# Optimization experiments

Hardware: AMD Instinct MI355X
Metric: run time of the kernel (lower is better)

Reference implementation:

```python
import math
import jax, jax.numpy as jnp
import numpy as np

B, LD, LE = 8, 512, 512
D, H, DK, F, L, V = 1024, 16, 64, 4096, 3, 32000
EPS = 1e-5
NEG = -1000000000.0


def setup_inputs() -> dict:
    key = jax.random.key(0)
    ks = jax.random.split(key, 16)
    s = 0.02
    dec_inputs = jax.random.randint(ks[0], (B, LD), 0, V)
    # causal mask: True = masked out (matches masked_fill semantics)
    self_mask = jnp.broadcast_to(jnp.triu(jnp.ones((LD, LD), bool), k=1), (B, LD, LD))
    enc_output = jax.random.normal(ks[1], (B, LE, D), jnp.float32)
    encoder_mask = jnp.zeros((B, LD, LE), bool)  # no encoder padding
    embed = jax.random.normal(ks[2], (V, D), jnp.float32) * s
    # sinusoidal positional encoding, pe[:LD]
    pos = jnp.arange(LD, dtype=jnp.float32)[:, None]
    div = jnp.exp(jnp.arange(0, D, 2, dtype=jnp.float32) * (-math.log(10000.0) / D))
    pe = jnp.zeros((LD, D), jnp.float32)
    pe = pe.at[:, 0::2].set(jnp.sin(pos * div)).at[:, 1::2].set(jnp.cos(pos * div))
    # per-layer params; axis 1 of attn params: 0=self-attn, 1=enc-dec attn
    wq = jax.random.normal(ks[3], (L, 2, D, D), jnp.float32) * s
    wk = jax.random.normal(ks[4], (L, 2, D, D), jnp.float32) * s
    wv = jax.random.normal(ks[5], (L, 2, D, D), jnp.float32) * s
    wo = jax.random.normal(ks[6], (L, 2, D, D), jnp.float32) * s
    bq = jnp.zeros((L, 2, D), jnp.float32)
    bk = jnp.zeros((L, 2, D), jnp.float32)
    bv = jnp.zeros((L, 2, D), jnp.float32)
    bo = jnp.zeros((L, 2, D), jnp.float32)
    ffn_w1 = jax.random.normal(ks[7], (L, F, D), jnp.float32) * s
    ffn_b1 = jnp.zeros((L, F), jnp.float32)
    ffn_w2 = jax.random.normal(ks[8], (L, D, F), jnp.float32) * s
    ffn_b2 = jnp.zeros((L, D), jnp.float32)
    ln_g = jnp.ones((L, 3, D), jnp.float32)   # norm1/2/3 gains
    ln_b = jnp.zeros((L, 3, D), jnp.float32)  # norm1/2/3 biases
    return dict(dec_inputs=dec_inputs, self_mask=self_mask, enc_output=enc_output,
                encoder_mask=encoder_mask, embed=embed, pe=pe,
                wq=wq, bq=bq, wk=wk, bk=bk, wv=wv, bv=bv, wo=wo, bo=bo,
                ffn_w1=ffn_w1, ffn_b1=ffn_b1, ffn_w2=ffn_w2, ffn_b2=ffn_b2,
                ln_g=ln_g, ln_b=ln_b)


def _ln(x, g, b):
    m = jnp.mean(x, axis=-1, keepdims=True)
    v = jnp.mean((x - m) ** 2, axis=-1, keepdims=True)
    return (x - m) * jax.lax.rsqrt(v + EPS) * g + b


def _mha(qi, ki, vi, mask, wq, bq, wk, bk, wv, bv, wo, bo):
    Bq, Lq, _ = qi.shape
    Lk = ki.shape[1]
    Q = (qi @ wq.T + bq).reshape(Bq, Lq, H, DK).transpose(0, 2, 1, 3)
    K = (ki @ wk.T + bk).reshape(Bq, Lk, H, DK).transpose(0, 2, 1, 3)
    Vv = (vi @ wv.T + bv).reshape(Bq, Lk, H, DK).transpose(0, 2, 1, 3)
    scores = jnp.einsum('bhqd,bhkd->bhqk', Q, K) / math.sqrt(DK)
    scores = jnp.where(mask[:, None, :, :], NEG, scores)
    attn = jax.nn.softmax(scores, axis=-1)
    ctx = jnp.einsum('bhqk,bhkd->bhqd', attn, Vv)
    ctx = ctx.transpose(0, 2, 1, 3).reshape(Bq, Lq, H * DK)
    return ctx @ wo.T + bo


def reference(dec_inputs, self_mask, enc_output, encoder_mask, embed, pe,
              wq, bq, wk, bk, wv, bv, wo, bo,
              ffn_w1, ffn_b1, ffn_w2, ffn_b2, ln_g, ln_b):
    x = embed[dec_inputs] * math.sqrt(D) + pe[None, :, :]
    for l in range(L):
        h = _ln(x, ln_g[l, 0], ln_b[l, 0])
        a = _mha(h, h, h, self_mask,
                 wq[l, 0], bq[l, 0], wk[l, 0], bk[l, 0], wv[l, 0], bv[l, 0], wo[l, 0], bo[l, 0])
        x = x + a
        h = _ln(x, ln_g[l, 1], ln_b[l, 1])
        c = _mha(h, enc_output, enc_output, encoder_mask,
                 wq[l, 1], bq[l, 1], wk[l, 1], bk[l, 1], wv[l, 1], bv[l, 1], wo[l, 1], bo[l, 1])
        x = x + c
        h = _ln(x, ln_g[l, 2], ln_b[l, 2])
        f = jax.nn.relu(h @ ffn_w1[l].T + ffn_b1[l]) @ ffn_w2[l].T + ffn_b2[l]
        # faithful quirk of the source: residual is the cross-attn output, not x
        x = c + f
    return x
```

## Files before the change

kernel.cpp:

```cpp
#include <hip/hip_runtime.h>
#include <hip/hip_bf16.h>

using bf16x8 = __attribute__((ext_vector_type(8))) short;
using f32x4  = __attribute__((ext_vector_type(4))) float;
using u16x4  = __attribute__((ext_vector_type(4))) unsigned short;

#define DEVI static __device__ __forceinline__
#define SBAR() asm volatile("s_barrier" ::: "memory")

DEVI unsigned short f2b(float f) {
  unsigned int u = __float_as_uint(f);
  u += 0x7FFFu + ((u >> 16) & 1u);
  return (unsigned short)(u >> 16);
}

DEVI void gload16(const unsigned short* g, unsigned short* l) {
  __builtin_amdgcn_global_load_lds(
      (const __attribute__((address_space(1))) unsigned int*)g,
      (__attribute__((address_space(3))) unsigned int*)l, 16, 0, 0);
}

DEVI float wred_max16(float v) {
#pragma unroll
  for (int m = 1; m < 16; m <<= 1) v = fmaxf(v, __shfl_xor(v, m, 64));
  return v;
}
DEVI float wred_sum16(float v) {
#pragma unroll
  for (int m = 1; m < 16; m <<= 1) v += __shfl_xor(v, m, 64);
  return v;
}


__global__ void cvt_kernel(const float* __restrict__ in,
                           unsigned short* __restrict__ out, int n4) {
  int i = blockIdx.x * blockDim.x + threadIdx.x;
  const int stride = gridDim.x * blockDim.x;
  for (; i < n4; i += stride) {
    const float4 v = ((const float4*)in)[i];
    u16x4 o;
    o[0] = f2b(v.x); o[1] = f2b(v.y); o[2] = f2b(v.z); o[3] = f2b(v.w);
    ((u16x4*)out)[i] = o;
  }
}

__global__ void pack_w(const float* __restrict__ s0,
                       const float* __restrict__ s1,
                       const float* __restrict__ s2,
                       int sub, unsigned short* __restrict__ dst, int nm) {
  const int r = blockIdx.x;
  const int m = blockIdx.y;
  const int l = blockIdx.z;
  const float* src = (m == 0 ? s0 : m == 1 ? s1 : s2)
                   + (size_t)(l * 2 + sub) * 1048576 + (size_t)r * 1024;
  unsigned short* d = dst + ((size_t)(l * nm + m) * 1024 + r) * 1024;
  const int col = threadIdx.x * 4;
  const float4 v = *(const float4*)(src + col);
  u16x4 o;
  o[0] = f2b(v.x); o[1] = f2b(v.y); o[2] = f2b(v.z); o[3] = f2b(v.w);
  *(u16x4*)(d + col) = o;
}

__global__ void pack_bias(const float* __restrict__ s0,
                          const float* __restrict__ s1,
                          const float* __restrict__ s2,
                          int sub, float* __restrict__ dst, int nm) {
  const int m = blockIdx.x, l = blockIdx.y;
  const float* src = (m == 0 ? s0 : m == 1 ? s1 : s2) + (size_t)(l * 2 + sub) * 1024;
  float* d = dst + ((size_t)l * nm + m) * 1024;
  const int i = threadIdx.x * 4;
  *(float4*)(d + i) = *(const float4*)(src + i);
}

__global__ void embed_kernel(const int* __restrict__ ids,
                             const float* __restrict__ emb,
                             const float* __restrict__ pe,
                             float* __restrict__ x) {
  const int row = blockIdx.x;
  const int t = row & 511;
  const int col = threadIdx.x * 4;
  const int id = ids[row];
  const float4 e = *(const float4*)(emb + (size_t)id * 1024 + col);
  const float4 p = *(const float4*)(pe + (size_t)t * 1024 + col);
  float4 o;
  o.x = e.x * 32.f + p.x; o.y = e.y * 32.f + p.y;
  o.z = e.z * 32.f + p.z; o.w = e.w * 32.f + p.w;
  *(float4*)(x + (size_t)row * 1024 + col) = o;
}

__global__ void ln_kernel(const float* __restrict__ x,
                          const float* __restrict__ g,
                          const float* __restrict__ b,
                          unsigned short* __restrict__ out) {
  const int row = blockIdx.x;
  const int l = threadIdx.x;
  const float4* xr = (const float4*)(x + (size_t)row * 1024);
  float4 v[4];
  float s = 0.f;
#pragma unroll
  for (int i = 0; i < 4; ++i) {
    v[i] = xr[l * 4 + i];
    s += v[i].x + v[i].y + v[i].z + v[i].w;
  }
#pragma unroll
  for (int m = 1; m < 64; m <<= 1) s += __shfl_xor(s, m, 64);
  const float mean = s * (1.f / 1024.f);
  float vs = 0.f;
#pragma unroll
  for (int i = 0; i < 4; ++i) {
    float dx = v[i].x - mean, dy = v[i].y - mean, dz = v[i].z - mean, dw = v[i].w - mean;
    vs += dx * dx + dy * dy + dz * dz + dw * dw;
  }
#pragma unroll
  for (int m = 1; m < 64; m <<= 1) vs += __shfl_xor(vs, m, 64);
  const float inv = rsqrtf(vs * (1.f / 1024.f) + 1e-5f);
#pragma unroll
  for (int i = 0; i < 4; ++i) {
    const int col = l * 16 + i * 4;
    const float4 gg = *(const float4*)(g + col);
    const float4 bb = *(const float4*)(b + col);
    u16x4 o;
    o[0] = f2b((v[i].x - mean) * inv * gg.x + bb.x);
    o[1] = f2b((v[i].y - mean) * inv * gg.y + bb.y);
    o[2] = f2b((v[i].z - mean) * inv * gg.z + bb.z);
    o[3] = f2b((v[i].w - mean) * inv * gg.w + bb.w);
    *(u16x4*)(out + (size_t)row * 1024 + col) = o;
  }
}

__global__ void reduce4_ln_kernel(const float* __restrict__ c,
                                  const float* __restrict__ pbuf,
                                  const float* __restrict__ bias,
                                  const float* __restrict__ g,
                                  const float* __restrict__ e,
                                  float* __restrict__ x,
                                  unsigned short* __restrict__ hb) {
  const int row = blockIdx.x;
  const int l = threadIdx.x;
  const size_t base = (size_t)row * 1024;
  const float4* cc = (const float4*)(c + base);
  const float4* p0 = (const float4*)(pbuf + base);
  const float4* p1 = (const float4*)(pbuf + 4194304 + base);
  const float4* p2 = (const float4*)(pbuf + 2 * 4194304 + base);
  const float4* p3 = (const float4*)(pbuf + 3 * 4194304 + base);
  float4 v[4];
  float s = 0.f;
#pragma unroll
  for (int i = 0; i < 4; ++i) {
    const int fi = l * 4 + i;
    const float4 a = cc[fi];
    const float4 b0 = p0[fi], b1 = p1[fi], b2v = p2[fi], b3 = p3[fi];
    const float4 bb = ((const float4*)bias)[fi & 255];
    float4 o;
    o.x = a.x + (b0.x + b1.x) + (b2v.x + b3.x) + bb.x;
    o.y = a.y + (b0.y + b1.y) + (b2v.y + b3.y) + bb.y;
    o.z = a.z + (b0.z + b1.z) + (b2v.z + b3.z) + bb.z;
    o.w = a.w + (b0.w + b1.w) + (b2v.w + b3.w) + bb.w;
    v[i] = o;
    s += o.x + o.y + o.z + o.w;
    *(float4*)(x + base + fi * 4) = o;
  }
#pragma unroll
  for (int m = 1; m < 64; m <<= 1) s += __shfl_xor(s, m, 64);
  const float mean = s * (1.f / 1024.f);
  float vs = 0.f;
#pragma unroll
  for (int i = 0; i < 4; ++i) {
    float dx = v[i].x - mean, dy = v[i].y - mean, dz = v[i].z - mean, dw = v[i].w - mean;
    vs += dx * dx + dy * dy + dz * dz + dw * dw;
  }
#pragma unroll
  for (int m = 1; m < 64; m <<= 1) vs += __shfl_xor(vs, m, 64);
  const float inv = rsqrtf(vs * (1.f / 1024.f) + 1e-5f);
#pragma unroll
  for (int i = 0; i < 4; ++i) {
    const int col = l * 16 + i * 4;
    const float4 gg = *(const float4*)(g + col);
    const float4 bb = *(const float4*)(e + col);
    u16x4 o;
    o[0] = f2b((v[i].x - mean) * inv * gg.x + bb.x);
    o[1] = f2b((v[i].y - mean) * inv * gg.y + bb.y);
    o[2] = f2b((v[i].z - mean) * inv * gg.z + bb.z);
    o[3] = f2b((v[i].w - mean) * inv * gg.w + bb.w);
    *(u16x4*)(hb + base + col) = o;
  }
}


template<int LDA, int LDB>
DEVI void gemm8p_core(const unsigned short* __restrict__ A,
                      const unsigned short* __restrict__ Bw,
                      int m0, int n0, int kofs,
                      unsigned short* AsE, unsigned short* BsE,
                      unsigned short* AsO, unsigned short* BsO,
                      int tid, f32x4 (&acc)[8][4]) {
  constexpr int NT = 16;
  const int lane = tid & 63;
  const int wave = tid >> 6;
  const int wr = wave >> 2;
  const int wc = wave & 3;
  const int ro = lane & 15;
  const int hi = lane >> 4;

  auto stA = [&](unsigned short* buf, int q, int kt) {
    const int row = tid >> 3;
    const int lc = (tid & 7) ^ (row & 7);
    gload16(A + (size_t)(m0 + q * 64 + row) * LDA + kofs + kt * 64 + lc * 8,
            buf + q * 4096 + tid * 8);
  };
  auto stB = [&](unsigned short* buf, int q, int kt) {
    const int row = tid >> 3;
    const int lc = (tid & 7) ^ (row & 7);
    gload16(Bw + (size_t)(n0 + q * 64 + row) * LDB + kofs + kt * 64 + lc * 8,
            buf + q * 4096 + tid * 8);
  };

  bf16x8 af[4][2], bfL[2][2], bfR[2][2];
  auto ldAL = [&](const unsigned short* buf) {
#pragma unroll
    for (int mi = 0; mi < 4; ++mi) {
      const int r = wr * 128 + mi * 16 + ro;
#pragma unroll
      for (int ks = 0; ks < 2; ++ks)
        af[mi][ks] = *(const bf16x8*)&buf[r * 64 + (((ks << 2) + hi) ^ (r & 7)) * 8];
    }
  };
  auto ldAH = [&](const unsigned short* buf) {
#pragma unroll
    for (int mi = 0; mi < 4; ++mi) {
      const int r = wr * 128 + 64 + mi * 16 + ro;
#pragma unroll
      for (int ks = 0; ks < 2; ++ks)
        af[mi][ks] = *(const bf16x8*)&buf[r * 64 + (((ks << 2) + hi) ^ (r & 7)) * 8];
    }
  };
  auto ldBL = [&](const unsigned short* buf) {
#pragma unroll
    for (int nj = 0; nj < 2; ++nj) {
      const int r = wc * 64 + nj * 16 + ro;
#pragma unroll
      for (int ks = 0; ks < 2; ++ks)
        bfL[nj][ks] = *(const bf16x8*)&buf[r * 64 + (((ks << 2) + hi) ^ (r & 7)) * 8];
    }
  };
  auto ldBR = [&](const unsigned short* buf) {
#pragma unroll
    for (int nj = 0; nj < 2; ++nj) {
      const int r = wc * 64 + 32 + nj * 16 + ro;
#pragma unroll
      for (int ks = 0; ks < 2; ++ks)
        bfR[nj][ks] = *(const bf16x8*)&buf[r * 64 + (((ks << 2) + hi) ^ (r & 7)) * 8];
    }
  };
  auto mmQ = [&](bf16x8 (&bf)[2][2], int mo, int no) {
    __builtin_amdgcn_s_setprio(1);
#pragma unroll
    for (int ks = 0; ks < 2; ++ks)
#pragma unroll
      for (int mi = 0; mi < 4; ++mi)
#pragma unroll
        for (int nj = 0; nj < 2; ++nj)
          acc[mo + mi][no + nj] =
              __builtin_amdgcn_mfma_f32_16x16x32_bf16(af[mi][ks], bf[nj][ks],
                                                      acc[mo + mi][no + nj], 0, 0, 0);
    __builtin_amdgcn_s_setprio(0);
  };

  stA(AsE, 0, 0); stA(AsE, 1, 0); stA(AsE, 2, 0); stA(AsE, 3, 0);
  stB(BsE, 0, 0); stB(BsE, 1, 0); stB(BsE, 2, 0); stB(BsE, 3, 0);
  stA(AsO, 0, 1); stA(AsO, 1, 1); stA(AsO, 2, 1); stA(AsO, 3, 1);
  stB(BsO, 0, 1); stB(BsO, 1, 1);
  asm volatile("s_waitcnt vmcnt(0)" ::: "memory");
  SBAR();

  for (int t = 0; t < NT; t += 2) {
    const bool last = (t + 2 >= NT);
    ldAL(AsE); ldBL(BsE);
    stB(BsO, 2, t + 1); stB(BsO, 3, t + 1);
    SBAR(); mmQ(bfL, 0, 0); SBAR();
    ldBR(BsE);
    if (!last) { stA(AsE, 0, t + 2); stA(AsE, 2, t + 2); }
    SBAR(); mmQ(bfR, 0, 2); SBAR();
    ldAH(AsE);
    if (!last) { stB(BsE, 0, t + 2); stB(BsE, 1, t + 2); }
    SBAR(); mmQ(bfL, 4, 0); SBAR();
    if (!last) {
      stA(AsE, 1, t + 2); stA(AsE, 3, t + 2);
      asm volatile("s_waitcnt vmcnt(6)" ::: "memory");
    } else {
      asm volatile("s_waitcnt vmcnt(0)" ::: "memory");
    }
    SBAR(); mmQ(bfR, 4, 2); SBAR();
    ldAL(AsO); ldBL(BsO);
    if (!last) { stB(BsE, 2, t + 2); stB(BsE, 3, t + 2); }
    SBAR(); mmQ(bfL, 0, 0); SBAR();
    ldBR(BsO);
    if (!last) { stA(AsO, 0, t + 3); stA(AsO, 2, t + 3); }
    SBAR(); mmQ(bfR, 0, 2); SBAR();
    ldAH(AsO);
    if (!last) { stB(BsO, 0, t + 3); stB(BsO, 1, t + 3); }
    SBAR(); mmQ(bfL, 4, 0); SBAR();
    if (!last) {
      stA(AsO, 1, t + 3); stA(AsO, 3, t + 3);
      asm volatile("s_waitcnt vmcnt(6)" ::: "memory");
    }
    SBAR(); mmQ(bfR, 4, 2); SBAR();
  }
}

template<int EPI, int VT>
__global__ __launch_bounds__(512, 1) void gemm8p(
    const unsigned short* __restrict__ A,
    const unsigned short* __restrict__ Bw,
    const float* __restrict__ bias,
    int N, unsigned short* __restrict__ out0,
    unsigned short* __restrict__ vt) {
  __shared__ alignas(16) unsigned short AsE[256 * 64];
  __shared__ alignas(16) unsigned short BsE[256 * 64];
  __shared__ alignas(16) unsigned short AsO[256 * 64];
  __shared__ alignas(16) unsigned short BsO[256 * 64];
  const int tid = threadIdx.x;
  int id = blockIdx.x;
  const int nwg = gridDim.x;
  id = (id & 7) * (nwg >> 3) + (id >> 3);
  const int nn = N >> 8;
  const int bx = id % nn;
  const int by = id / nn;
  const int m0 = by * 256;
  const int n0 = bx * 256;

  f32x4 acc[8][4];
#pragma unroll
  for (int i = 0; i < 8; ++i)
#pragma unroll
    for (int j = 0; j < 4; ++j) acc[i][j] = f32x4{0.f, 0.f, 0.f, 0.f};

  gemm8p_core<1024, 1024>(A, Bw, m0, n0, 0, AsE, BsE, AsO, BsO, tid, acc);

  const int lane = tid & 63;
  const int wave = tid >> 6;
  const int wr = wave >> 2, wc = wave & 3;
  const int ro = lane & 15, hi = lane >> 4;
  const int r4 = hi * 4;
#pragma unroll
  for (int mi = 0; mi < 8; ++mi) {
#pragma unroll
    for (int nj = 0; nj < 4; ++nj) {
      const int cg = n0 + wc * 64 + nj * 16 + ro;
      const float bv = bias[cg];
      const int rg0 = m0 + wr * 128 + mi * 16 + r4;
      const bool isV1 = (VT == 1) && (cg >= 2048);
      const bool isV2 = (VT == 2) && ((cg & 2047) >= 1024);
      if (isV1 || isV2) {
        u16x4 o;
#pragma unroll
        for (int q = 0; q < 4; ++q) o[q] = f2b(acc[mi][nj][q] + bv);
        const int b = rg0 >> 9, t = rg0 & 511;
        size_t dst;
        if (isV1) {
          const int hh = (cg - 2048) >> 6, d = (cg - 2048) & 63;
          dst = (((size_t)(b * 16 + hh) * 64 + d) << 9) + t;
        } else {
          const int layer = cg >> 11;
          const int cm = (cg & 2047) - 1024;
          dst = (size_t)layer * 4194304 +
                (((size_t)(b * 16 + (cm >> 6)) * 64 + (cm & 63)) << 9) + t;
        }
        *(u16x4*)&vt[dst] = o;
      } else {
#pragma unroll
        for (int q = 0; q < 4; ++q) {
          const float v = acc[mi][nj][q] + bv;
          out0[(size_t)(rg0 + q) * N + cg] = f2b(EPI == 1 ? fmaxf(v, 0.f) : v);
        }
      }
    }
  }
}

__global__ __launch_bounds__(512, 1) void gemm_sk8(
    const unsigned short* __restrict__ A,
    const unsigned short* __restrict__ Bw,
    float* __restrict__ pbuf) {
  __shared__ alignas(16) unsigned short AsE[256 * 64];
  __shared__ alignas(16) unsigned short BsE[256 * 64];
  __shared__ alignas(16) unsigned short AsO[256 * 64];
  __shared__ alignas(16) unsigned short BsO[256 * 64];
  const int tid = threadIdx.x;
  int id = blockIdx.x;
  const int nwg = gridDim.x;
  id = (id & 7) * (nwg >> 3) + (id >> 3);
  const int s  = id >> 6;
  const int r6 = id & 63;
  const int bx = r6 & 3;
  const int by = r6 >> 2;
  const int m0 = by * 256;
  const int n0 = bx * 256;

  f32x4 acc[8][4];
#pragma unroll
  for (int i = 0; i < 8; ++i)
#pragma unroll
    for (int j = 0; j < 4; ++j) acc[i][j] = f32x4{0.f, 0.f, 0.f, 0.f};

  gemm8p_core<4096, 4096>(A, Bw, m0, n0, s * 1024, AsE, BsE, AsO, BsO, tid, acc);

  float* out = pbuf + (size_t)s * 4096 * 1024;
  const int lane = tid & 63;
  const int wave = tid >> 6;
  const int wr = wave >> 2, wc = wave & 3;
  const int ro = lane & 15, hi = lane >> 4;
  const int r4 = hi * 4;
#pragma unroll
  for (int mi = 0; mi < 8; ++mi)
#pragma unroll
    for (int nj = 0; nj < 4; ++nj) {
      const int cg = n0 + wc * 64 + nj * 16 + ro;
#pragma unroll
      for (int q = 0; q < 4; ++q) {
        const int rg = m0 + wr * 128 + mi * 16 + r4 + q;
        out[(size_t)rg * 1024 + cg] = acc[mi][nj][q];
      }
    }
}

__global__ void reduce4_kernel(const float* __restrict__ c,
                               const float* __restrict__ pbuf,
                               const float* __restrict__ bias,
                               float* __restrict__ xout) {
  const int n4 = 4096 * 1024 / 4;
  int i = blockIdx.x * blockDim.x + threadIdx.x;
  const int stride = gridDim.x * blockDim.x;
  const float4* p0 = (const float4*)pbuf;
  const float4* p1 = (const float4*)(pbuf + 4194304);
  const float4* p2 = (const float4*)(pbuf + 2 * 4194304);
  const float4* p3 = (const float4*)(pbuf + 3 * 4194304);
  for (; i < n4; i += stride) {
    const float4 cc = ((const float4*)c)[i];
    const float4 a0 = p0[i];
    const float4 a1 = p1[i];
    const float4 a2 = p2[i];
    const float4 a3 = p3[i];
    const float4 bb = ((const float4*)bias)[i & 255];
    float4 o;
    o.x = cc.x + (a0.x + a1.x) + (a2.x + a3.x) + bb.x;
    o.y = cc.y + (a0.y + a1.y) + (a2.y + a3.y) + bb.y;
    o.z = cc.z + (a0.z + a1.z) + (a2.z + a3.z) + bb.z;
    o.w = cc.w + (a0.w + a1.w) + (a2.w + a3.w) + bb.w;
    ((float4*)xout)[i] = o;
  }
}


enum { EPI_BF16 = 0, EPI_RELU_BF16 = 1, EPI_RES = 2, EPI_RES2 = 3 };

template<int EPI, int BM, int BN>
__global__ void gemm_bt(const unsigned short* __restrict__ A,
                        const unsigned short* __restrict__ Bw,
                        const float* __restrict__ bias,
                        int N, int K, int nn,
                        void* out0, const float* res, float* out1) {
  constexpr int MI = BM / 32;
  constexpr int NJ = BN / 32;
  __shared__ alignas(16) unsigned short As[2][BM * 64];
  __shared__ alignas(16) unsigned short Bs[2][BN * 64];
  const int tid = threadIdx.x;
  const int lane = tid & 63;
  const int wave = tid >> 6;
  int id = blockIdx.x;
  const int nwg = gridDim.x;
  id = (id & 7) * (nwg >> 3) + (id >> 3);
  const int bx = id % nn;
  const int by = id / nn;
  const int m0 = by * BM;
  const int n0 = bx * BN;
  const int wm = (wave >> 1) * (BM / 2);
  const int wn = (wave & 1) * (BN / 2);

  auto stage = [&](int buf, int kt) {
    const size_t k0 = (size_t)kt * 64;
#pragma unroll
    for (int i = 0; i < MI; ++i) {
      const int c = tid + 256 * i;
      const int row = c >> 3;
      const int lc = (c & 7) ^ (row & 7);
      gload16(A + (size_t)(m0 + row) * K + k0 + lc * 8, &As[buf][c * 8]);
    }
#pragma unroll
    for (int i = 0; i < NJ; ++i) {
      const int c = tid + 256 * i;
      const int row = c >> 3;
      const int lc = (c & 7) ^ (row & 7);
      gload16(Bw + (size_t)(n0 + row) * K + k0 + lc * 8, &Bs[buf][c * 8]);
    }
  };

  f32x4 acc[MI][NJ];
#pragma unroll
  for (int i = 0; i < MI; ++i)
#pragma unroll
    for (int j = 0; j < NJ; ++j) acc[i][j] = f32x4{0.f, 0.f, 0.f, 0.f};

  const int nk = K >> 6;
  stage(0, 0);
  int cur = 0;
  const int ro = lane & 15;
  const int hi = lane >> 4;
  for (int kt = 0; kt < nk; ++kt) {
    __syncthreads();
    if (kt + 1 < nk) stage(cur ^ 1, kt + 1);
    bf16x8 af[MI][2], bf[NJ][2];
#pragma unroll
    for (int i = 0; i < MI; ++i) {
      const int r = wm + i * 16 + ro;
#pragma unroll
      for (int ks = 0; ks < 2; ++ks)
        af[i][ks] = *(const bf16x8*)&As[cur][r * 64 + (((ks << 2) + hi) ^ (r & 7)) * 8];
    }
#pragma unroll
    for (int j = 0; j < NJ; ++j) {
      const int r = wn + j * 16 + ro;
#pragma unroll
      for (int ks = 0; ks < 2; ++ks)
        bf[j][ks] = *(const bf16x8*)&Bs[cur][r * 64 + (((ks << 2) + hi) ^ (r & 7)) * 8];
    }
#pragma unroll
    for (int ks = 0; ks < 2; ++ks)
#pragma unroll
      for (int i = 0; i < MI; ++i)
#pragma unroll
        for (int j = 0; j < NJ; ++j)
          acc[i][j] = __builtin_amdgcn_mfma_f32_16x16x32_bf16(af[i][ks], bf[j][ks], acc[i][j], 0, 0, 0);
    cur ^= 1;
  }

  const int r4 = hi * 4;
#pragma unroll
  for (int i = 0; i < MI; ++i) {
#pragma unroll
    for (int j = 0; j < NJ; ++j) {
      const int cg = n0 + wn + j * 16 + ro;
      const float bv = bias[cg];
#pragma unroll
      for (int q = 0; q < 4; ++q) {
        const int rg = m0 + wm + i * 16 + r4 + q;
        const size_t idx = (size_t)rg * N + cg;
        const float v = acc[i][j][q] + bv;
        if (EPI == EPI_BF16) {
          ((unsigned short*)out0)[idx] = f2b(v);
        } else if (EPI == EPI_RELU_BF16) {
          ((unsigned short*)out0)[idx] = f2b(fmaxf(v, 0.f));
        } else if (EPI == EPI_RES) {
          ((float*)out0)[idx] = res[idx] + v;
        } else {
          const float r = res[idx];
          ((float*)out0)[idx] = v;
          out1[idx] = r + v;
        }
      }
    }
  }
}


template<bool CAUSAL>
__global__ __launch_bounds__(256) void attn_kernel(
    const unsigned short* __restrict__ Qg, int qs,
    const unsigned short* __restrict__ Kg, int ksd,
    const unsigned short* __restrict__ Vt,
    unsigned short* __restrict__ Og) {
  __shared__ alignas(16) unsigned short Ks[2][64 * 64];
  __shared__ alignas(16) unsigned short Vs[2][64 * 64];
  __shared__ alignas(16) unsigned short Pl[4][32 * 64];
  const int qt0 = blockIdx.x;
  const int h  = blockIdx.y;
  const int b  = blockIdx.z;
  const int tid = threadIdx.x;
  const int lane = tid & 63;
  const int w = tid >> 6;
  const int ro = lane & 15;
  const int hi = lane >> 4;
  const int qrow0 = qt0 * 128 + w * 32;
  const size_t qbase = (size_t)b * 512 * qs  + (size_t)h * 64;
  const size_t kbase = (size_t)b * 512 * ksd + (size_t)h * 64;
  const size_t vbase = ((size_t)(b * 16 + h)) * 64 * 512;
  const size_t obase = (size_t)b * 512 * 1024 + (size_t)h * 64;

  bf16x8 qf[2][2];
#pragma unroll
  for (int mi = 0; mi < 2; ++mi)
#pragma unroll
    for (int ks = 0; ks < 2; ++ks)
      qf[mi][ks] = *(const bf16x8*)&Qg[qbase + (size_t)(qrow0 + mi * 16 + ro) * qs + ks * 32 + hi * 8];

  f32x4 o[2][4];
  float mrun[2][4], lrun[2][4];
#pragma unroll
  for (int mi = 0; mi < 2; ++mi) {
#pragma unroll
    for (int di = 0; di < 4; ++di) o[mi][di] = f32x4{0.f, 0.f, 0.f, 0.f};
#pragma unroll
    for (int q = 0; q < 4; ++q) { mrun[mi][q] = -1e30f; lrun[mi][q] = 0.f; }
  }

  auto stage = [&](int buf, int kt) {
#pragma unroll
    for (int i = 0; i < 2; ++i) {
      const int c = tid + 256 * i;
      const int row = c >> 3;
      const int lc = (c & 7) ^ (row & 7);
      gload16(Kg + kbase + (size_t)(kt * 64 + row) * ksd + lc * 8, &Ks[buf][c * 8]);
    }
#pragma unroll
    for (int i = 0; i < 2; ++i) {
      const int c = tid + 256 * i;
      const int row = c >> 3;
      const int lc = (c & 7) ^ (row & 7);
      gload16(Vt + vbase + (size_t)row * 512 + (size_t)kt * 64 + lc * 8, &Vs[buf][c * 8]);
    }
  };

  const int ktmax = CAUSAL ? (qt0 * 2 + 1) : 7;
  stage(0, 0);
  int cur = 0;
  for (int kt = 0; kt <= ktmax; ++kt) {
    __syncthreads();
    if (kt < ktmax) stage(cur ^ 1, kt + 1);
    const bool skip = CAUSAL && (kt * 64 > qrow0 + 31);
    if (!skip) {
      bf16x8 kf[4][2];
#pragma unroll
      for (int ni = 0; ni < 4; ++ni) {
        const int r = ni * 16 + ro;
#pragma unroll
        for (int ks = 0; ks < 2; ++ks)
          kf[ni][ks] = *(const bf16x8*)&Ks[cur][r * 64 + (((ks << 2) + hi) ^ (r & 7)) * 8];
      }

      f32x4 s[2][4];
#pragma unroll
      for (int mi = 0; mi < 2; ++mi)
#pragma unroll
        for (int ni = 0; ni < 4; ++ni) s[mi][ni] = f32x4{0.f, 0.f, 0.f, 0.f};
#pragma unroll
      for (int ks = 0; ks < 2; ++ks)
#pragma unroll
        for (int mi = 0; mi < 2; ++mi)
#pragma unroll
          for (int ni = 0; ni < 4; ++ni)
            s[mi][ni] = __builtin_amdgcn_mfma_f32_16x16x32_bf16(qf[mi][ks], kf[ni][ks], s[mi][ni], 0, 0, 0);

      const bool dm = CAUSAL && (kt * 64 + 63 > qrow0);
#pragma unroll
      for (int mi = 0; mi < 2; ++mi)
#pragma unroll
        for (int ni = 0; ni < 4; ++ni)
#pragma unroll
          for (int q = 0; q < 4; ++q) {
            float e = s[mi][ni][q] * 0.125f;
            if (dm && (kt * 64 + ni * 16 + ro) > (qrow0 + mi * 16 + hi * 4 + q)) e = -1e9f;
            s[mi][ni][q] = e;
          }

      float fac[2][4];
#pragma unroll
      for (int mi = 0; mi < 2; ++mi)
#pragma unroll
        for (int q = 0; q < 4; ++q) {
          float rm = s[mi][0][q];
#pragma unroll
          for (int ni = 1; ni < 4; ++ni) rm = fmaxf(rm, s[mi][ni][q]);
          rm = wred_max16(rm);
          const float mn = fmaxf(mrun[mi][q], rm);
          fac[mi][q] = __expf(mrun[mi][q] - mn);
          mrun[mi][q] = mn;
        }
#pragma unroll
      for (int mi = 0; mi < 2; ++mi)
#pragma unroll
        for (int q = 0; q < 4; ++q) {
          float rs = 0.f;
#pragma unroll
          for (int ni = 0; ni < 4; ++ni) {
            const float pv = __expf(s[mi][ni][q] - mrun[mi][q]);
            s[mi][ni][q] = pv;
            rs += pv;
          }
          rs = wred_sum16(rs);
          lrun[mi][q] = lrun[mi][q] * fac[mi][q] + rs;
        }
#pragma unroll
      for (int mi = 0; mi < 2; ++mi)
#pragma unroll
        for (int di = 0; di < 4; ++di)
#pragma unroll
          for (int q = 0; q < 4; ++q) o[mi][di][q] *= fac[mi][q];

#pragma unroll
      for (int mi = 0; mi < 2; ++mi)
#pragma unroll
        for (int ni = 0; ni < 4; ++ni)
#pragma unroll
          for (int q = 0; q < 4; ++q) {
            const int row = mi * 16 + hi * 4 + q;
            const int col = ni * 16 + ro;
            const int sc  = ((col >> 3) ^ (row & 7)) * 8 + (col & 7);
            Pl[w][row * 64 + sc] = f2b(s[mi][ni][q]);
          }

      bf16x8 pa[2][2];
#pragma unroll
      for (int mi = 0; mi < 2; ++mi)
#pragma unroll
        for (int ks = 0; ks < 2; ++ks) {
          const int row = mi * 16 + ro;
          pa[mi][ks] = *(const bf16x8*)&Pl[w][row * 64 + (((ks << 2) + hi) ^ (row & 7)) * 8];
        }

#pragma unroll
      for (int di = 0; di < 4; ++di)
#pragma unroll
        for (int ks = 0; ks < 2; ++ks) {
          const int r = di * 16 + ro;
          const bf16x8 vf = *(const bf16x8*)&Vs[cur][r * 64 + (((ks << 2) + hi) ^ (r & 7)) * 8];
#pragma unroll
          for (int mi = 0; mi < 2; ++mi)
            o[mi][di] = __builtin_amdgcn_mfma_f32_16x16x32_bf16(pa[mi][ks], vf, o[mi][di], 0, 0, 0);
        }
    }
    cur ^= 1;
  }

#pragma unroll
  for (int mi = 0; mi < 2; ++mi)
#pragma unroll
    for (int di = 0; di < 4; ++di)
#pragma unroll
      for (int q = 0; q < 4; ++q) {
        const float val = o[mi][di][q] / lrun[mi][q];
        Og[obase + (size_t)(qrow0 + mi * 16 + hi * 4 + q) * 1024 + di * 16 + ro] = f2b(val);
      }
}


extern "C" void kernel_launch(void* const* d_in, const int* in_sizes, int n_in,
                              void* d_out, int out_size, void* d_ws, size_t ws_size,
                              hipStream_t stream) {
  (void)in_sizes; (void)n_in; (void)out_size; (void)ws_size;
  const int*   dec = (const int*)d_in[0];
  const float* enc = (const float*)d_in[2];
  const float* emb = (const float*)d_in[4];
  const float* pe  = (const float*)d_in[5];
  const float* wq  = (const float*)d_in[6];
  const float* bq  = (const float*)d_in[7];
  const float* wk  = (const float*)d_in[8];
  const float* bk  = (const float*)d_in[9];
  const float* wv  = (const float*)d_in[10];
  const float* bv  = (const float*)d_in[11];
  const float* wo  = (const float*)d_in[12];
  const float* bo  = (const float*)d_in[13];
  const float* w1  = (const float*)d_in[14];
  const float* b1  = (const float*)d_in[15];
  const float* w2  = (const float*)d_in[16];
  const float* b2  = (const float*)d_in[17];
  const float* lng = (const float*)d_in[18];
  const float* lnb = (const float*)d_in[19];

  const size_t SZ_ACT = 4194304ull;

  char* p = (char*)d_ws;
  auto alloc = [&](size_t bytes) { char* r = p; p += (bytes + 255) & ~(size_t)255; return r; };
  unsigned short* qkvw  = (unsigned short*)alloc(3ull * 3 * 1048576 * 2);
  unsigned short* kvw   = (unsigned short*)alloc(3ull * 2 * 1048576 * 2);
  unsigned short* wqxb  = (unsigned short*)alloc(3ull * 1048576 * 2);
  unsigned short* Wob   = (unsigned short*)alloc(6291456ull * 2);
  unsigned short* W1b   = (unsigned short*)alloc(12582912ull * 2);
  unsigned short* W2b   = (unsigned short*)alloc(12582912ull * 2);
  unsigned short* encb  = (unsigned short*)alloc(SZ_ACT * 2);
  float*          x     = (float*)alloc(SZ_ACT * 4);
  float*          c     = (float*)alloc(SZ_ACT * 4);
  unsigned short* hb    = (unsigned short*)alloc(SZ_ACT * 2);
  unsigned short* qkvb  = (unsigned short*)alloc(4096ull * 3072 * 2);
  unsigned short* kvb   = (unsigned short*)alloc(4096ull * 6144 * 2);
  unsigned short* qb    = (unsigned short*)alloc(SZ_ACT * 2);
  unsigned short* vtbS  = (unsigned short*)alloc(SZ_ACT * 2);
  unsigned short* vtb3  = (unsigned short*)alloc(3ull * SZ_ACT * 2);
  unsigned short* mid   = (unsigned short*)alloc(4096ull * 4096 * 2);
  float*          pbuf  = (float*)alloc(4ull * SZ_ACT * 4);
  float*          qkvbias = (float*)alloc(3ull * 3072 * 4);
  float*          kvbias  = (float*)alloc(3ull * 2048 * 4);

  cvt_kernel<<<2048, 256, 0, stream>>>(wo, Wob, 1572864);
  cvt_kernel<<<2048, 256, 0, stream>>>(w1, W1b, 3145728);
  cvt_kernel<<<2048, 256, 0, stream>>>(w2, W2b, 3145728);
  cvt_kernel<<<2048, 256, 0, stream>>>(enc, encb, 1048576);
  pack_w<<<dim3(1024, 3, 3), 256, 0, stream>>>(wq, wk, wv, 0, qkvw, 3);
  pack_w<<<dim3(1024, 2, 3), 256, 0, stream>>>(wk, wv, wv, 1, kvw, 2);
  pack_w<<<dim3(1024, 1, 3), 256, 0, stream>>>(wq, wq, wq, 1, wqxb, 1);
  pack_bias<<<dim3(3, 3), 256, 0, stream>>>(bq, bk, bv, 0, qkvbias, 3);
  pack_bias<<<dim3(2, 3), 256, 0, stream>>>(bk, bv, bv, 1, kvbias, 2);
  embed_kernel<<<4096, 256, 0, stream>>>(dec, emb, pe, x);

  gemm8p<0, 2><<<16 * 24, 512, 0, stream>>>(encb, kvw, kvbias, 6144, kvb, vtb3);

  const dim3 gAttn(4, 16, 8);

  for (int l = 0; l < 3; ++l) {
    const float* g0 = lng + (l * 3 + 0) * 1024; const float* e0 = lnb + (l * 3 + 0) * 1024;
    const float* g1 = lng + (l * 3 + 1) * 1024; const float* e1 = lnb + (l * 3 + 1) * 1024;
    const float* g2 = lng + (l * 3 + 2) * 1024; const float* e2 = lnb + (l * 3 + 2) * 1024;

    if (l == 0)
      ln_kernel<<<4096, 64, 0, stream>>>(x, g0, e0, hb);
    gemm8p<0, 1><<<16 * 12, 512, 0, stream>>>(hb, qkvw + (size_t)l * 3 * 1048576,
        qkvbias + l * 3072, 3072, qkvb, vtbS);
    attn_kernel<true><<<gAttn, 256, 0, stream>>>(qkvb, 3072, qkvb + 1024, 3072, vtbS, hb);
    gemm_bt<EPI_RES, 128, 64><<<32 * 16, 256, 0, stream>>>(hb, Wob + (size_t)(l * 2) * 1048576,
        bo + (l * 2) * 1024, 1024, 1024, 16, x, x, nullptr);

    ln_kernel<<<4096, 64, 0, stream>>>(x, g1, e1, hb);
    gemm_bt<EPI_BF16, 128, 64><<<32 * 16, 256, 0, stream>>>(hb, wqxb + (size_t)l * 1048576,
        bq + (l * 2 + 1) * 1024, 1024, 1024, 16, qb, nullptr, nullptr);
    attn_kernel<false><<<gAttn, 256, 0, stream>>>(qb, 1024, kvb + l * 2048, 6144,
        vtb3 + (size_t)l * SZ_ACT, hb);
    gemm_bt<EPI_RES2, 128, 64><<<32 * 16, 256, 0, stream>>>(hb, Wob + (size_t)(l * 2 + 1) * 1048576,
        bo + (l * 2 + 1) * 1024, 1024, 1024, 16, c, x, x);

    ln_kernel<<<4096, 64, 0, stream>>>(x, g2, e2, hb);
    gemm8p<1, 0><<<16 * 16, 512, 0, stream>>>(hb, W1b + (size_t)l * 4194304,
        b1 + l * 4096, 4096, mid, nullptr);
    gemm_sk8<<<256, 512, 0, stream>>>(mid, W2b + (size_t)l * 4194304, pbuf);
    if (l == 2) {
      reduce4_kernel<<<2048, 256, 0, stream>>>(c, pbuf, b2 + l * 1024, (float*)d_out);
    } else {
      const float* gn = lng + ((l + 1) * 3 + 0) * 1024;
      const float* en = lnb + ((l + 1) * 3 + 0) * 1024;
      reduce4_ln_kernel<<<4096, 64, 0, stream>>>(c, pbuf, b2 + l * 1024, gn, en, x, hb);
    }
  }
}
```

Measured before the change: 1.073 ms.

## Replace 128x64 GEMM with 128x128 tile, quarter-staged software-pipelined kernel

Swaps the double-buffered 128x64 GEMM used for the attention output and cross-attention query projections for a new 128x128-tile kernel. The new kernel splits each K-tile load into quarter chunks interleaved with half-tile MFMA phases, uses explicit vmcnt waits and barriers, and raises wave priority around MFMA blocks. The goal is to overlap global-to-LDS loads with compute and raise reuse per tile. The cost is half as many workgroups (256 on a GPU with many CUs), which may leave the device under-filled, plus more complex synchronisation.

```diff
diff --git a/kernel.cpp b/kernel.cpp
--- a/kernel.cpp
+++ b/kernel.cpp
@@ -454,98 +454,127 @@
 
 enum { EPI_BF16 = 0, EPI_RELU_BF16 = 1, EPI_RES = 2, EPI_RES2 = 3 };
 
-template<int EPI, int BM, int BN>
-__global__ void gemm_bt(const unsigned short* __restrict__ A,
-                        const unsigned short* __restrict__ Bw,
-                        const float* __restrict__ bias,
-                        int N, int K, int nn,
-                        void* out0, const float* res, float* out1) {
-  constexpr int MI = BM / 32;
-  constexpr int NJ = BN / 32;
-  __shared__ alignas(16) unsigned short As[2][BM * 64];
-  __shared__ alignas(16) unsigned short Bs[2][BN * 64];
+template<int EPI>
+__global__ __launch_bounds__(256, 2) void gemm_s8(
+    const unsigned short* __restrict__ A,
+    const unsigned short* __restrict__ Bw,
+    const float* __restrict__ bias,
+    int N, int K, int nn,
+    void* out0, const float* res, float* out1) {
+  __shared__ alignas(16) unsigned short AsE[128 * 64];
+  __shared__ alignas(16) unsigned short BsE[128 * 64];
+  __shared__ alignas(16) unsigned short AsO[128 * 64];
+  __shared__ alignas(16) unsigned short BsO[128 * 64];
   const int tid = threadIdx.x;
   const int lane = tid & 63;
   const int wave = tid >> 6;
+  const int wr = wave >> 1;
+  const int wc = wave & 1;
   int id = blockIdx.x;
   const int nwg = gridDim.x;
   id = (id & 7) * (nwg >> 3) + (id >> 3);
   const int bx = id % nn;
   const int by = id / nn;
-  const int m0 = by * BM;
-  const int n0 = bx * BN;
-  const int wm = (wave >> 1) * (BM / 2);
-  const int wn = (wave & 1) * (BN / 2);
-
-  auto stage = [&](int buf, int kt) {
-    const size_t k0 = (size_t)kt * 64;
-#pragma unroll
-    for (int i = 0; i < MI; ++i) {
-      const int c = tid + 256 * i;
-      const int row = c >> 3;
-      const int lc = (c & 7) ^ (row & 7);
-      gload16(A + (size_t)(m0 + row) * K + k0 + lc * 8, &As[buf][c * 8]);
-    }
-#pragma unroll
-    for (int i = 0; i < NJ; ++i) {
-      const int c = tid + 256 * i;
-      const int row = c >> 3;
-      const int lc = (c & 7) ^ (row & 7);
-      gload16(Bw + (size_t)(n0 + row) * K + k0 + lc * 8, &Bs[buf][c * 8]);
-    }
-  };
-
-  f32x4 acc[MI][NJ];
-#pragma unroll
-  for (int i = 0; i < MI; ++i)
-#pragma unroll
-    for (int j = 0; j < NJ; ++j) acc[i][j] = f32x4{0.f, 0.f, 0.f, 0.f};
-
-  const int nk = K >> 6;
-  stage(0, 0);
-  int cur = 0;
+  const int m0 = by * 128;
+  const int n0 = bx * 128;
   const int ro = lane & 15;
   const int hi = lane >> 4;
-  for (int kt = 0; kt < nk; ++kt) {
-    __syncthreads();
-    if (kt + 1 < nk) stage(cur ^ 1, kt + 1);
-    bf16x8 af[MI][2], bf[NJ][2];
-#pragma unroll
-    for (int i = 0; i < MI; ++i) {
-      const int r = wm + i * 16 + ro;
+
+  auto stA = [&](unsigned short* buf, int q, int kt) {
+    const int row = q * 32 + (tid >> 3);
+    const int lc = (tid & 7) ^ (row & 7);
+    gload16(A + (size_t)(m0 + row) * K + (size_t)kt * 64 + lc * 8,
+            buf + q * 2048 + tid * 8);
+  };
+  auto stB = [&](unsigned short* buf, int q, int kt) {
+    const int row = q * 32 + (tid >> 3);
+    const int lc = (tid & 7) ^ (row & 7);
+    gload16(Bw + (size_t)(n0 + row) * K + (size_t)kt * 64 + lc * 8,
+            buf + q * 2048 + tid * 8);
+  };
+
+  f32x4 acc[4][4];
+#pragma unroll
+  for (int i = 0; i < 4; ++i)
+#pragma unroll
+    for (int j = 0; j < 4; ++j) acc[i][j] = f32x4{0.f, 0.f, 0.f, 0.f};
+
+  bf16x8 af[2][2], bf[4][2];
+  auto ldA = [&](const unsigned short* buf, int half) {
+#pragma unroll
+    for (int mi = 0; mi < 2; ++mi) {
+      const int r = wr * 64 + (half * 2 + mi) * 16 + ro;
 #pragma unroll
       for (int ks = 0; ks < 2; ++ks)
-        af[i][ks] = *(const bf16x8*)&As[cur][r * 64 + (((ks << 2) + hi) ^ (r & 7)) * 8];
-    }
-#pragma unroll
-    for (int j = 0; j < NJ; ++j) {
-      const int r = wn + j * 16 + ro;
+        af[mi][ks] = *(const bf16x8*)&buf[r * 64 + (((ks << 2) + hi) ^ (r & 7)) * 8];
+    }
+  };
+  auto ldB = [&](const unsigned short* buf) {
+#pragma unroll
+    for (int nj = 0; nj < 4; ++nj) {
+      const int r = wc * 64 + nj * 16 + ro;
 #pragma unroll
       for (int ks = 0; ks < 2; ++ks)
-        bf[j][ks] = *(const bf16x8*)&Bs[cur][r * 64 + (((ks << 2) + hi) ^ (r & 7)) * 8];
-    }
+        bf[nj][ks] = *(const bf16x8*)&buf[r * 64 + (((ks << 2) + hi) ^ (r & 7)) * 8];
+    }
+  };
+  auto mmH = [&](int half) {
+    __builtin_amdgcn_s_setprio(1);
 #pragma unroll
     for (int ks = 0; ks < 2; ++ks)
 #pragma unroll
-      for (int i = 0; i < MI; ++i)
-#pragma unroll
-        for (int j = 0; j < NJ; ++j)
-          acc[i][j] = __builtin_amdgcn_mfma_f32_16x16x32_bf16(af[i][ks], bf[j][ks], acc[i][j], 0, 0, 0);
-    cur ^= 1;
+      for (int mi = 0; mi < 2; ++mi)
+#pragma unroll
+        for (int nj = 0; nj < 4; ++nj)
+          acc[half * 2 + mi][nj] =
+              __builtin_amdgcn_mfma_f32_16x16x32_bf16(af[mi][ks], bf[nj][ks],
+                                                      acc[half * 2 + mi][nj], 0, 0, 0);
+    __builtin_amdgcn_s_setprio(0);
+  };
+
+  const int NT = K >> 6;
+  stA(AsE, 0, 0); stA(AsE, 1, 0); stA(AsE, 2, 0); stA(AsE, 3, 0);
+  stB(BsE, 0, 0); stB(BsE, 1, 0); stB(BsE, 2, 0); stB(BsE, 3, 0);
+  stA(AsO, 0, 1); stA(AsO, 2, 1);
+  stB(BsO, 0, 1); stB(BsO, 1, 1);
+  asm volatile("s_waitcnt vmcnt(0)" ::: "memory");
+  SBAR();
+
+  for (int t = 0; t < NT; t += 2) {
+    const bool last = (t + 2 >= NT);
+    ldA(AsE, 0); ldB(BsE);
+    stB(BsO, 2, t + 1); stB(BsO, 3, t + 1);
+    stA(AsO, 1, t + 1); stA(AsO, 3, t + 1);
+    SBAR(); mmH(0); SBAR();
+    ldA(AsE, 1);
+    if (!last) { stA(AsE, 0, t + 2); stA(AsE, 2, t + 2);
+                 stB(BsE, 0, t + 2); stB(BsE, 1, t + 2); }
+    if (!last) asm volatile("s_waitcnt vmcnt(4)" ::: "memory");
+    else       asm volatile("s_waitcnt vmcnt(0)" ::: "memory");
+    SBAR(); mmH(1); SBAR();
+    ldA(AsO, 0); ldB(BsO);
+    if (!last) { stA(AsE, 1, t + 2); stA(AsE, 3, t + 2);
+                 stB(BsE, 2, t + 2); stB(BsE, 3, t + 2); }
+    SBAR(); mmH(0); SBAR();
+    ldA(AsO, 1);
+    if (!last) { stA(AsO, 0, t + 3); stA(AsO, 2, t + 3);
+                 stB(BsO, 0, t + 3); stB(BsO, 1, t + 3); }
+    if (!last) asm volatile("s_waitcnt vmcnt(4)" ::: "memory");
+    SBAR(); mmH(1); SBAR();
   }
 
   const int r4 = hi * 4;
 #pragma unroll
-  for (int i = 0; i < MI; ++i) {
-#pragma unroll
-    for (int j = 0; j < NJ; ++j) {
-      const int cg = n0 + wn + j * 16 + ro;
+  for (int mi = 0; mi < 4; ++mi) {
+#pragma unroll
+    for (int nj = 0; nj < 4; ++nj) {
+      const int cg = n0 + wc * 64 + nj * 16 + ro;
       const float bv = bias[cg];
 #pragma unroll
       for (int q = 0; q < 4; ++q) {
-        const int rg = m0 + wm + i * 16 + r4 + q;
+        const int rg = m0 + wr * 64 + mi * 16 + r4 + q;
         const size_t idx = (size_t)rg * N + cg;
-        const float v = acc[i][j][q] + bv;
+        const float v = acc[mi][nj][q] + bv;
         if (EPI == EPI_BF16) {
           ((unsigned short*)out0)[idx] = f2b(v);
         } else if (EPI == EPI_RELU_BF16) {
@@ -815,16 +844,16 @@
     gemm8p<0, 1><<<16 * 12, 512, 0, stream>>>(hb, qkvw + (size_t)l * 3 * 1048576,
         qkvbias + l * 3072, 3072, qkvb, vtbS);
     attn_kernel<true><<<gAttn, 256, 0, stream>>>(qkvb, 3072, qkvb + 1024, 3072, vtbS, hb);
-    gemm_bt<EPI_RES, 128, 64><<<32 * 16, 256, 0, stream>>>(hb, Wob + (size_t)(l * 2) * 1048576,
-        bo + (l * 2) * 1024, 1024, 1024, 16, x, x, nullptr);
+    gemm_s8<EPI_RES><<<32 * 8, 256, 0, stream>>>(hb, Wob + (size_t)(l * 2) * 1048576,
+        bo + (l * 2) * 1024, 1024, 1024, 8, x, x, nullptr);
 
     ln_kernel<<<4096, 64, 0, stream>>>(x, g1, e1, hb);
-    gemm_bt<EPI_BF16, 128, 64><<<32 * 16, 256, 0, stream>>>(hb, wqxb + (size_t)l * 1048576,
-        bq + (l * 2 + 1) * 1024, 1024, 1024, 16, qb, nullptr, nullptr);
+    gemm_s8<EPI_BF16><<<32 * 8, 256, 0, stream>>>(hb, wqxb + (size_t)l * 1048576,
+        bq + (l * 2 + 1) * 1024, 1024, 1024, 8, qb, nullptr, nullptr);
     attn_kernel<false><<<gAttn, 256, 0, stream>>>(qb, 1024, kvb + l * 2048, 6144,
         vtb3 + (size_t)l * SZ_ACT, hb);
-    gemm_bt<EPI_RES2, 128, 64><<<32 * 16, 256, 0, stream>>>(hb, Wob + (size_t)(l * 2 + 1) * 1048576,
-        bo + (l * 2 + 1) * 1024, 1024, 1024, 16, c, x, x);
+    gemm_s8<EPI_RES2><<<32 * 8, 256, 0, stream>>>(hb, Wob + (size_t)(l * 2 + 1) * 1048576,
+        bo + (l * 2 + 1) * 1024, 1024, 1024, 8, c, x, x);
 
     ln_kernel<<<4096, 64, 0, stream>>>(x, g2, e2, hb);
     gemm8p<1, 0><<<16 * 16, 512, 0, stream>>>(hb, W1b + (size_t)l * 4194304,
```

Result: slower. 1.113 ms (+3.8%).
